# Optimization experiments

Measured on AMD Instinct MI355X. Metric: run time of the kernel, lower is better.

## Reference

```python
import jax, jax.numpy as jnp
import numpy as np

N_NODES = 50000
N_EDGES = 600000
LATENT = 128
IN_FEAT = 7
STEPS = 3
MLP_LAYERS = 2


def setup_inputs() -> dict:
    key = jax.random.key(0)
    ks = jax.random.split(key, 8)
    s = 0.05
    nodes = jax.random.normal(ks[0], (N_NODES, IN_FEAT), jnp.float32)
    senders = jax.random.randint(ks[1], (N_EDGES,), 0, N_NODES, jnp.int32)
    receivers = jax.random.randint(ks[2], (N_EDGES,), 0, N_NODES, jnp.int32)
    W_embed = jax.random.normal(ks[3], (IN_FEAT, LATENT), jnp.float32) * s
    b_embed = jnp.zeros((LATENT,), jnp.float32)
    mlp_W = jax.random.normal(ks[4], (STEPS, MLP_LAYERS, LATENT, LATENT), jnp.float32) * s
    mlp_b = jnp.zeros((STEPS, MLP_LAYERS, LATENT), jnp.float32)
    ln_scale = jnp.ones((STEPS, LATENT), jnp.float32)
    ln_bias = jnp.zeros((STEPS, LATENT), jnp.float32)
    W_dec = jax.random.normal(ks[5], (LATENT, IN_FEAT), jnp.float32) * s
    b_dec = jnp.zeros((IN_FEAT,), jnp.float32)
    return dict(nodes=nodes, senders=senders, receivers=receivers,
                W_embed=W_embed, b_embed=b_embed, mlp_W=mlp_W, mlp_b=mlp_b,
                ln_scale=ln_scale, ln_bias=ln_bias, W_dec=W_dec, b_dec=b_dec)


def _layer_norm(x, scale, bias, eps=1e-6):
    mu = jnp.mean(x, axis=-1, keepdims=True)
    var = jnp.var(x, axis=-1, keepdims=True)
    return (x - mu) * jax.lax.rsqrt(var + eps) * scale + bias


def reference(nodes, senders, receivers, W_embed, b_embed, mlp_W, mlp_b,
              ln_scale, ln_bias, W_dec, b_dec):
    n = nodes.shape[0]
    # symmetric normalization factors (jraph GraphConvolution default)
    ones = jnp.ones((senders.shape[0],), dtype=nodes.dtype)
    sender_deg = jax.ops.segment_sum(ones, senders, num_segments=n)
    receiver_deg = jax.ops.segment_sum(ones, receivers, num_segments=n)
    inv_sqrt_s = jax.lax.rsqrt(jnp.maximum(sender_deg, 1.0))[:, None]
    inv_sqrt_r = jax.lax.rsqrt(jnp.maximum(receiver_deg, 1.0))[:, None]

    # node embedder
    h = nodes @ W_embed + b_embed  # [N, LATENT]
    for step in range(mlp_W.shape[0]):
        # per-node MLP update (update_node_fn applied before aggregation)
        x = h
        for l in range(mlp_W.shape[1]):
            x = jax.nn.relu(x @ mlp_W[step, l] + mlp_b[step, l])
        # normalized gather -> scatter-sum aggregation
        x = x * inv_sqrt_s
        x = jax.ops.segment_sum(x[senders], receivers, num_segments=n)
        x = x * inv_sqrt_r
        # skip connection + layer norm
        h = _layer_norm(h + x, ln_scale[step], ln_bias[step])
    # decoder back to input feature size
    return h @ W_dec + b_dec  # [N, IN_FEAT]
```

## Files before the change

kernel.cpp:

```cpp
#include <hip/hip_runtime.h>

#define NN 50000
#define NE 600000
#define LAT 128
#define IN_F 7
#define CSR_W 64
#define HSTR 136
#define NXCD 8
#define RNG (NN / NXCD)

typedef __attribute__((ext_vector_type(8))) short bfrag;
typedef __attribute__((ext_vector_type(4))) float ffrag;
typedef __attribute__((ext_vector_type(2))) float f32x2;

__device__ inline unsigned short f2bf(float f) {
    unsigned int u = __float_as_uint(f);
    return (unsigned short)((u + 0x7FFFu + ((u >> 16) & 1u)) >> 16);
}
__device__ inline float bf2f(unsigned int b) { return __uint_as_float(b << 16); }


__global__ void k_prep(const float* __restrict__ W, unsigned short* __restrict__ Wp,
                       unsigned int* __restrict__ cnt) {
    int t = blockIdx.x * 256 + threadIdx.x;
    if (t < NN) cnt[t] = 0;
    if (t < 6 * 8 * 4 * 64) {
        int lane = t & 63;
        int ks = (t >> 6) & 3;
        int nt = (t >> 8) & 7;
        int mat = t >> 11;
        int n = nt * 16 + (lane & 15);
        int k0 = ks * 32 + (lane >> 4) * 8;
        const float* src = W + (size_t)mat * LAT * LAT;
        unsigned long long lo = 0, hi = 0;
#pragma unroll
        for (int j = 0; j < 4; ++j)
            lo |= (unsigned long long)f2bf(src[(k0 + j) * LAT + n]) << (16 * j);
#pragma unroll
        for (int j = 0; j < 4; ++j)
            hi |= (unsigned long long)f2bf(src[(k0 + 4 + j) * LAT + n]) << (16 * j);
        unsigned long long* dst = (unsigned long long*)(Wp + (size_t)t * 8);
        dst[0] = lo; dst[1] = hi;
    }
}


__global__ __launch_bounds__(256) void k_fused1(
    const int* __restrict__ s, const int* __restrict__ r,
    unsigned int* __restrict__ cnt, unsigned short* __restrict__ slot,
    const float* __restrict__ nodes, const float* __restrict__ We,
    const float* __restrict__ be,
    const unsigned short* __restrict__ W0p, const unsigned short* __restrict__ W1p,
    const float* __restrict__ b0, const float* __restrict__ b1,
    unsigned char* __restrict__ x, int build_blocks)
{
    __shared__ unsigned short hs[64][HSTR];
    int tid = threadIdx.x;

    if ((int)blockIdx.x < build_blocks) {
        int g = blockIdx.x & (NXCD - 1);
        int stripe = blockIdx.x >> 3;
        int i = stripe * 256 + tid;
        if (i < NE) {
            int ss = s[i], rr = r[i];
            int rlo = g * RNG;
            if (ss >= rlo && ss < rlo + RNG)
                atomicAdd(&cnt[ss], 1u);
            if (rr >= rlo && rr < rlo + RNG) {
                unsigned int p = atomicAdd(&cnt[rr], 0x10000u) >> 16;
                if (p < CSR_W) slot[(size_t)rr * CSR_W + p] = (unsigned short)ss;
            }
        }
        return;
    }

    int brow = ((int)blockIdx.x - build_blocks) * 64;
    int rows = NN - brow; if (rows > 64) rows = 64;

#pragma unroll
    for (int it = 0; it < 8; ++it) {
        int fi = it * 256 + tid;
        int rr = fi >> 5, cc = (fi & 31) << 2;
        if (rr < rows) {
            const float* nr = nodes + (size_t)(brow + rr) * IN_F;
            float o0 = be[cc], o1 = be[cc + 1], o2 = be[cc + 2], o3 = be[cc + 3];
#pragma unroll
            for (int k = 0; k < IN_F; ++k) {
                float nv = nr[k];
                const float* wk = We + k * LAT + cc;
                o0 += nv * wk[0]; o1 += nv * wk[1];
                o2 += nv * wk[2]; o3 += nv * wk[3];
            }
            unsigned long long pk = (unsigned long long)f2bf(o0)
                | ((unsigned long long)f2bf(o1) << 16)
                | ((unsigned long long)f2bf(o2) << 32)
                | ((unsigned long long)f2bf(o3) << 48);
            *(unsigned long long*)&hs[rr][cc] = pk;
        }
    }
    __syncthreads();

    int w = tid >> 6, lane = tid & 63;
    int mrow = w * 16 + (lane & 15);
    int koff = (lane >> 4) * 8;
    int ccol = lane & 15;
    int crow = w * 16 + (lane >> 4) * 4;

    float bia0[8], bia1[8];
#pragma unroll
    for (int nt = 0; nt < 8; ++nt) { bia0[nt] = b0[nt * 16 + ccol]; bia1[nt] = b1[nt * 16 + ccol]; }

    ffrag acc[8];
#pragma unroll
    for (int nt = 0; nt < 8; ++nt) acc[nt] = (ffrag)0.0f;
#pragma unroll
    for (int ks = 0; ks < 4; ++ks) {
        bfrag af = *(const bfrag*)&hs[mrow][ks * 32 + koff];
#pragma unroll
        for (int nt = 0; nt < 8; ++nt) {
            bfrag bf = *(const bfrag*)&W0p[(size_t)(((nt * 4) + ks) * 64 + lane) * 8];
            acc[nt] = __builtin_amdgcn_mfma_f32_16x16x32_bf16(af, bf, acc[nt], 0, 0, 0);
        }
    }
#pragma unroll
    for (int nt = 0; nt < 8; ++nt)
#pragma unroll
        for (int reg = 0; reg < 4; ++reg)
            hs[crow + reg][nt * 16 + ccol] = f2bf(fmaxf(acc[nt][reg] + bia0[nt], 0.f));
    __syncthreads();

#pragma unroll
    for (int nt = 0; nt < 8; ++nt) acc[nt] = (ffrag)0.0f;
#pragma unroll
    for (int ks = 0; ks < 4; ++ks) {
        bfrag af = *(const bfrag*)&hs[mrow][ks * 32 + koff];
#pragma unroll
        for (int nt = 0; nt < 8; ++nt) {
            bfrag bf = *(const bfrag*)&W1p[(size_t)(((nt * 4) + ks) * 64 + lane) * 8];
            acc[nt] = __builtin_amdgcn_mfma_f32_16x16x32_bf16(af, bf, acc[nt], 0, 0, 0);
        }
    }
    __syncthreads();
#pragma unroll
    for (int nt = 0; nt < 8; ++nt)
#pragma unroll
        for (int reg = 0; reg < 4; ++reg)
            hs[crow + reg][nt * 16 + ccol] = f2bf(fmaxf(acc[nt][reg] + bia1[nt], 0.f));
    __syncthreads();

#pragma unroll
    for (int it = 0; it < 8; ++it) {
        int fi = it * 256 + tid;
        int rr = fi >> 5, uc = fi & 31;
        if (rr < rows) {
            unsigned long long pk8 = *(unsigned long long*)&hs[rr][uc * 4];
            float f0 = bf2f((unsigned int)(pk8 & 0xFFFFu));
            float f1 = bf2f((unsigned int)((pk8 >> 16) & 0xFFFFu));
            float f2 = bf2f((unsigned int)((pk8 >> 32) & 0xFFFFu));
            float f3 = bf2f((unsigned int)((pk8 >> 48) & 0xFFFFu));
            int o = __builtin_amdgcn_cvt_pk_fp8_f32(f0, f1, 0, false);
            o = __builtin_amdgcn_cvt_pk_fp8_f32(f2, f3, o, true);
            *(int*)&x[(size_t)(brow + rr) * LAT + uc * 4] = o;
        }
    }
}


__global__ __launch_bounds__(256) void k_mlp2(
    const unsigned short* __restrict__ h,
    const unsigned short* __restrict__ W0p, const unsigned short* __restrict__ W1p,
    const float* __restrict__ b0, const float* __restrict__ b1,
    const unsigned int* __restrict__ cnt,
    unsigned char* __restrict__ x, int M)
{
    __shared__ unsigned short hs[64][HSTR];
    int brow = blockIdx.x * 64;
    int tid = threadIdx.x;
    int rows = M - brow; if (rows > 64) rows = 64;

#pragma unroll
    for (int it = 0; it < 8; ++it) {
        int fi = it * 256 + tid;
        int rr = fi >> 5, cc = (fi & 31) << 2;
        if (rr < rows)
            *(unsigned long long*)&hs[rr][cc] =
                *(const unsigned long long*)&h[(size_t)(brow + rr) * LAT + cc];
    }
    __syncthreads();

    int w = tid >> 6, lane = tid & 63;
    int mrow = w * 16 + (lane & 15);
    int koff = (lane >> 4) * 8;
    int ccol = lane & 15;
    int crow = w * 16 + (lane >> 4) * 4;

    float bia0[8], bia1[8];
#pragma unroll
    for (int nt = 0; nt < 8; ++nt) { bia0[nt] = b0[nt * 16 + ccol]; bia1[nt] = b1[nt * 16 + ccol]; }
    float iv[4];
#pragma unroll
    for (int reg = 0; reg < 4; ++reg) {
        int rw = brow + crow + reg;
        unsigned int ds = cnt[rw < NN ? rw : NN - 1] & 0xFFFFu;
        iv[reg] = rsqrtf((float)(ds > 1 ? ds : 1));
    }

    ffrag acc[8];
#pragma unroll
    for (int nt = 0; nt < 8; ++nt) acc[nt] = (ffrag)0.0f;
#pragma unroll
    for (int ks = 0; ks < 4; ++ks) {
        bfrag af = *(const bfrag*)&hs[mrow][ks * 32 + koff];
#pragma unroll
        for (int nt = 0; nt < 8; ++nt) {
            bfrag bf = *(const bfrag*)&W0p[(size_t)(((nt * 4) + ks) * 64 + lane) * 8];
            acc[nt] = __builtin_amdgcn_mfma_f32_16x16x32_bf16(af, bf, acc[nt], 0, 0, 0);
        }
    }
#pragma unroll
    for (int nt = 0; nt < 8; ++nt)
#pragma unroll
        for (int reg = 0; reg < 4; ++reg)
            hs[crow + reg][nt * 16 + ccol] = f2bf(fmaxf(acc[nt][reg] + bia0[nt], 0.f));
    __syncthreads();

#pragma unroll
    for (int nt = 0; nt < 8; ++nt) acc[nt] = (ffrag)0.0f;
#pragma unroll
    for (int ks = 0; ks < 4; ++ks) {
        bfrag af = *(const bfrag*)&hs[mrow][ks * 32 + koff];
#pragma unroll
        for (int nt = 0; nt < 8; ++nt) {
            bfrag bf = *(const bfrag*)&W1p[(size_t)(((nt * 4) + ks) * 64 + lane) * 8];
            acc[nt] = __builtin_amdgcn_mfma_f32_16x16x32_bf16(af, bf, acc[nt], 0, 0, 0);
        }
    }
    __syncthreads();
#pragma unroll
    for (int nt = 0; nt < 8; ++nt)
#pragma unroll
        for (int reg = 0; reg < 4; ++reg)
            hs[crow + reg][nt * 16 + ccol] =
                f2bf(fmaxf(acc[nt][reg] + bia1[nt], 0.f) * iv[reg]);
    __syncthreads();

#pragma unroll
    for (int it = 0; it < 8; ++it) {
        int fi = it * 256 + tid;
        int rr = fi >> 5, uc = fi & 31;
        if (rr < rows) {
            unsigned long long pk8 = *(unsigned long long*)&hs[rr][uc * 4];
            float f0 = bf2f((unsigned int)(pk8 & 0xFFFFu));
            float f1 = bf2f((unsigned int)((pk8 >> 16) & 0xFFFFu));
            float f2 = bf2f((unsigned int)((pk8 >> 32) & 0xFFFFu));
            float f3 = bf2f((unsigned int)((pk8 >> 48) & 0xFFFFu));
            int o = __builtin_amdgcn_cvt_pk_fp8_f32(f0, f1, 0, false);
            o = __builtin_amdgcn_cvt_pk_fp8_f32(f2, f3, o, true);
            *(int*)&x[(size_t)(brow + rr) * LAT + uc * 4] = o;
        }
    }
}


__global__ __launch_bounds__(256) void k_agg(
    const unsigned char* __restrict__ x, unsigned short* __restrict__ h,
    const float* __restrict__ nodes, const float* __restrict__ We,
    const float* __restrict__ be,
    const unsigned int* __restrict__ cnt, const unsigned short* __restrict__ slot,
    const float* __restrict__ gamma, const float* __restrict__ beta,
    const float* __restrict__ Wd, const float* __restrict__ bd,
    float* __restrict__ outd, int mode)
{
    int lane = threadIdx.x & 63;
    int r = blockIdx.x * 4 + (threadIdx.x >> 6);
    if (r >= NN) return;

    int ct = (int)(cnt[r] >> 16);
    float ir = rsqrtf((float)(ct > 1 ? ct : 1));
    int c = ct > CSR_W ? CSR_W : ct;

    int myidx = (lane < c) ? (int)slot[(size_t)r * CSR_W + lane] : 0;

    int j0 = lane * 2;
    float ax0 = 0.f, ay0 = 0.f, ax1 = 0.f, ay1 = 0.f;
    float ax2 = 0.f, ay2 = 0.f, ax3 = 0.f, ay3 = 0.f;
    float ax4 = 0.f, ay4 = 0.f, ax5 = 0.f, ay5 = 0.f;
    float ax6 = 0.f, ay6 = 0.f, ax7 = 0.f, ay7 = 0.f;
    int e = 0;

    if (mode == 0) {
        float myinv = 0.f;
        if (lane < c) {
            unsigned int ds = cnt[myidx] & 0xFFFFu;
            myinv = rsqrtf((float)(ds > 1 ? ds : 1));
        }
        for (; e + 8 <= c; e += 8) {
            int s0 = __shfl(myidx, e),     s1 = __shfl(myidx, e + 1);
            int s2 = __shfl(myidx, e + 2), s3 = __shfl(myidx, e + 3);
            int s4 = __shfl(myidx, e + 4), s5 = __shfl(myidx, e + 5);
            int s6 = __shfl(myidx, e + 6), s7 = __shfl(myidx, e + 7);
            float w0 = __shfl(myinv, e),     w1 = __shfl(myinv, e + 1);
            float w2 = __shfl(myinv, e + 2), w3 = __shfl(myinv, e + 3);
            float w4 = __shfl(myinv, e + 4), w5 = __shfl(myinv, e + 5);
            float w6 = __shfl(myinv, e + 6), w7 = __shfl(myinv, e + 7);
            unsigned short v0 = *(const unsigned short*)&x[(size_t)s0 * LAT + j0];
            unsigned short v1 = *(const unsigned short*)&x[(size_t)s1 * LAT + j0];
            unsigned short v2 = *(const unsigned short*)&x[(size_t)s2 * LAT + j0];
            unsigned short v3 = *(const unsigned short*)&x[(size_t)s3 * LAT + j0];
            unsigned short v4 = *(const unsigned short*)&x[(size_t)s4 * LAT + j0];
            unsigned short v5 = *(const unsigned short*)&x[(size_t)s5 * LAT + j0];
            unsigned short v6 = *(const unsigned short*)&x[(size_t)s6 * LAT + j0];
            unsigned short v7 = *(const unsigned short*)&x[(size_t)s7 * LAT + j0];
            f32x2 d0 = __builtin_amdgcn_cvt_pk_f32_fp8((int)v0, false);
            f32x2 d1 = __builtin_amdgcn_cvt_pk_f32_fp8((int)v1, false);
            f32x2 d2 = __builtin_amdgcn_cvt_pk_f32_fp8((int)v2, false);
            f32x2 d3 = __builtin_amdgcn_cvt_pk_f32_fp8((int)v3, false);
            f32x2 d4 = __builtin_amdgcn_cvt_pk_f32_fp8((int)v4, false);
            f32x2 d5 = __builtin_amdgcn_cvt_pk_f32_fp8((int)v5, false);
            f32x2 d6 = __builtin_amdgcn_cvt_pk_f32_fp8((int)v6, false);
            f32x2 d7 = __builtin_amdgcn_cvt_pk_f32_fp8((int)v7, false);
            ax0 += d0.x * w0; ay0 += d0.y * w0;
            ax1 += d1.x * w1; ay1 += d1.y * w1;
            ax2 += d2.x * w2; ay2 += d2.y * w2;
            ax3 += d3.x * w3; ay3 += d3.y * w3;
            ax4 += d4.x * w4; ay4 += d4.y * w4;
            ax5 += d5.x * w5; ay5 += d5.y * w5;
            ax6 += d6.x * w6; ay6 += d6.y * w6;
            ax7 += d7.x * w7; ay7 += d7.y * w7;
        }
        for (; e < c; ++e) {
            int s0 = __shfl(myidx, e);
            float w0 = __shfl(myinv, e);
            unsigned short v0 = *(const unsigned short*)&x[(size_t)s0 * LAT + j0];
            f32x2 d0 = __builtin_amdgcn_cvt_pk_f32_fp8((int)v0, false);
            ax0 += d0.x * w0; ay0 += d0.y * w0;
        }
    } else {
        for (; e + 8 <= c; e += 8) {
            int s0 = __shfl(myidx, e),     s1 = __shfl(myidx, e + 1);
            int s2 = __shfl(myidx, e + 2), s3 = __shfl(myidx, e + 3);
            int s4 = __shfl(myidx, e + 4), s5 = __shfl(myidx, e + 5);
            int s6 = __shfl(myidx, e + 6), s7 = __shfl(myidx, e + 7);
            unsigned short v0 = *(const unsigned short*)&x[(size_t)s0 * LAT + j0];
            unsigned short v1 = *(const unsigned short*)&x[(size_t)s1 * LAT + j0];
            unsigned short v2 = *(const unsigned short*)&x[(size_t)s2 * LAT + j0];
            unsigned short v3 = *(const unsigned short*)&x[(size_t)s3 * LAT + j0];
            unsigned short v4 = *(const unsigned short*)&x[(size_t)s4 * LAT + j0];
            unsigned short v5 = *(const unsigned short*)&x[(size_t)s5 * LAT + j0];
            unsigned short v6 = *(const unsigned short*)&x[(size_t)s6 * LAT + j0];
            unsigned short v7 = *(const unsigned short*)&x[(size_t)s7 * LAT + j0];
            f32x2 d0 = __builtin_amdgcn_cvt_pk_f32_fp8((int)v0, false);
            f32x2 d1 = __builtin_amdgcn_cvt_pk_f32_fp8((int)v1, false);
            f32x2 d2 = __builtin_amdgcn_cvt_pk_f32_fp8((int)v2, false);
            f32x2 d3 = __builtin_amdgcn_cvt_pk_f32_fp8((int)v3, false);
            f32x2 d4 = __builtin_amdgcn_cvt_pk_f32_fp8((int)v4, false);
            f32x2 d5 = __builtin_amdgcn_cvt_pk_f32_fp8((int)v5, false);
            f32x2 d6 = __builtin_amdgcn_cvt_pk_f32_fp8((int)v6, false);
            f32x2 d7 = __builtin_amdgcn_cvt_pk_f32_fp8((int)v7, false);
            ax0 += d0.x; ay0 += d0.y;  ax1 += d1.x; ay1 += d1.y;
            ax2 += d2.x; ay2 += d2.y;  ax3 += d3.x; ay3 += d3.y;
            ax4 += d4.x; ay4 += d4.y;  ax5 += d5.x; ay5 += d5.y;
            ax6 += d6.x; ay6 += d6.y;  ax7 += d7.x; ay7 += d7.y;
        }
        for (; e < c; ++e) {
            int s0 = __shfl(myidx, e);
            unsigned short v0 = *(const unsigned short*)&x[(size_t)s0 * LAT + j0];
            f32x2 d0 = __builtin_amdgcn_cvt_pk_f32_fp8((int)v0, false);
            ax0 += d0.x; ay0 += d0.y;
        }
    }

    float a0 = (((ax0 + ax1) + (ax2 + ax3)) + ((ax4 + ax5) + (ax6 + ax7))) * ir;
    float a1 = (((ay0 + ay1) + (ay2 + ay3)) + ((ay4 + ay5) + (ay6 + ay7))) * ir;

    float v0, v1;
    if (mode == 0) {
        float o0 = be[j0], o1 = be[j0 + 1];
#pragma unroll
        for (int k = 0; k < IN_F; ++k) {
            float nv = nodes[(size_t)r * IN_F + k];
            o0 += nv * We[k * LAT + j0];
            o1 += nv * We[k * LAT + j0 + 1];
        }
        v0 = o0 + a0; v1 = o1 + a1;
    } else {
        unsigned int hv = *(const unsigned int*)&h[(size_t)r * LAT + j0];
        v0 = bf2f(hv & 0xFFFFu) + a0;
        v1 = bf2f(hv >> 16) + a1;
    }

    float sum = v0 + v1, sq = v0 * v0 + v1 * v1;
#pragma unroll
    for (int m = 1; m <= 32; m <<= 1) {
        sum += __shfl_xor(sum, m);
        sq  += __shfl_xor(sq, m);
    }
    float mu = sum * (1.f / LAT);
    float rs = rsqrtf(sq * (1.f / LAT) - mu * mu + 1e-6f);

    float o0 = (v0 - mu) * rs * gamma[j0] + beta[j0];
    float o1 = (v1 - mu) * rs * gamma[j0 + 1] + beta[j0 + 1];

    if (mode < 2) {
        *(unsigned int*)&h[(size_t)r * LAT + j0] =
            (unsigned int)f2bf(o0) | ((unsigned int)f2bf(o1) << 16);
    } else {
        const float* wd0 = Wd + j0 * IN_F;
        const float* wd1 = Wd + (j0 + 1) * IN_F;
#pragma unroll
        for (int f = 0; f < IN_F; ++f) {
            float pv = o0 * wd0[f] + o1 * wd1[f];
#pragma unroll
            for (int m = 1; m <= 32; m <<= 1) pv += __shfl_xor(pv, m);
            if (lane == 0) outd[(size_t)r * IN_F + f] = pv + bd[f];
        }
    }
}


extern "C" void kernel_launch(void* const* d_in, const int* in_sizes, int n_in,
                              void* d_out, int out_size, void* d_ws, size_t ws_size,
                              hipStream_t stream)
{
    const float* nodes   = (const float*)d_in[0];
    const int*   senders = (const int*)d_in[1];
    const int*   recvs   = (const int*)d_in[2];
    const float* W_embed = (const float*)d_in[3];
    const float* b_embed = (const float*)d_in[4];
    const float* mlp_W   = (const float*)d_in[5];
    const float* mlp_b   = (const float*)d_in[6];
    const float* ln_s    = (const float*)d_in[7];
    const float* ln_b    = (const float*)d_in[8];
    const float* W_dec   = (const float*)d_in[9];
    const float* b_dec   = (const float*)d_in[10];
    float* out = (float*)d_out;

    char* p = (char*)d_ws;
    auto alloc = [&](size_t bytes) -> char* {
        char* q = p; p += (bytes + 255) & ~(size_t)255; return q;
    };
    unsigned short* h    = (unsigned short*)alloc((size_t)NN * LAT * 2);
    unsigned char*  x    = (unsigned char*)alloc((size_t)NN * LAT);
    unsigned short* Wp   = (unsigned short*)alloc((size_t)6 * LAT * LAT * 2);
    unsigned int* cnt    = (unsigned int*)alloc((size_t)NN * 4);
    unsigned short* slot = (unsigned short*)alloc((size_t)NN * CSR_W * 2);

    k_prep<<<(NN + 255) / 256, 256, 0, stream>>>(mlp_W, Wp, cnt);

    int build_blocks = NXCD * ((NE + 255) / 256);
    int mlp_blocks   = (NN + 63) / 64;
    int agg_blocks   = (NN + 3) / 4;

    const float* b0 = mlp_b;
    k_fused1<<<build_blocks + mlp_blocks, 256, 0, stream>>>(
        senders, recvs, cnt, slot, nodes, W_embed, b_embed,
        Wp, Wp + (size_t)LAT * LAT, b0, b0 + LAT, x, build_blocks);

    k_agg<<<agg_blocks, 256, 0, stream>>>(
        x, h, nodes, W_embed, b_embed, cnt, slot,
        ln_s, ln_b, nullptr, nullptr, nullptr, 0);

    k_mlp2<<<mlp_blocks, 256, 0, stream>>>(
        h, Wp + (size_t)2 * LAT * LAT, Wp + (size_t)3 * LAT * LAT,
        b0 + 2 * LAT, b0 + 3 * LAT, cnt, x, NN);
    k_agg<<<agg_blocks, 256, 0, stream>>>(
        x, h, nodes, W_embed, b_embed, cnt, slot,
        ln_s + LAT, ln_b + LAT, nullptr, nullptr, nullptr, 1);

    k_mlp2<<<mlp_blocks, 256, 0, stream>>>(
        h, Wp + (size_t)4 * LAT * LAT, Wp + (size_t)5 * LAT * LAT,
        b0 + 4 * LAT, b0 + 5 * LAT, cnt, x, NN);
    k_agg<<<agg_blocks, 256, 0, stream>>>(
        x, h, nodes, W_embed, b_embed, cnt, slot,
        ln_s + 2 * LAT, ln_b + 2 * LAT, W_dec, b_dec, out, 2);
}
```

Baseline: 315.1 us.

## Process two nodes per wavefront in aggregation with 4-byte fp8 gathers

Restructures the aggregation/layernorm kernel so each 64-lane wavefront handles two destination nodes, 32 lanes each, with every lane gathering 4 fp8 features (a 4-byte load) instead of 2 (a 2-byte load). Edge indices and weights are held in two registers per lane and broadcast with shuffles; the edge loop runs to the larger degree of the paired nodes and zero-weights missing entries. The goal is fewer, wider gather transactions per edge and half the wavefronts. In exchange, work is wasted when the paired degrees differ, and the early return for out-of-range rows is gone, which is safe only because NN is divisible by 8.

```diff
diff --git a/kernel.cpp b/kernel.cpp
--- a/kernel.cpp
+++ b/kernel.cpp
@@ -271,148 +271,110 @@
     const float* __restrict__ Wd, const float* __restrict__ bd,
     float* __restrict__ outd, int mode)
 {
-    int lane = threadIdx.x & 63;
-    int r = blockIdx.x * 4 + (threadIdx.x >> 6);
-    if (r >= NN) return;
+    int tid = threadIdx.x;
+    int wid = tid >> 6;
+    int lane = tid & 63;
+    int half = lane >> 5;
+    int li = lane & 31;
+    int r = blockIdx.x * 8 + wid * 2 + half;
+    int cb = li * 4;
 
     int ct = (int)(cnt[r] >> 16);
     float ir = rsqrtf((float)(ct > 1 ? ct : 1));
     int c = ct > CSR_W ? CSR_W : ct;
 
-    int myidx = (lane < c) ? (int)slot[(size_t)r * CSR_W + lane] : 0;
-
-    int j0 = lane * 2;
-    float ax0 = 0.f, ay0 = 0.f, ax1 = 0.f, ay1 = 0.f;
-    float ax2 = 0.f, ay2 = 0.f, ax3 = 0.f, ay3 = 0.f;
-    float ax4 = 0.f, ay4 = 0.f, ax5 = 0.f, ay5 = 0.f;
-    float ax6 = 0.f, ay6 = 0.f, ax7 = 0.f, ay7 = 0.f;
-    int e = 0;
-
+    int idx0 = 0, idx1 = 0;
+    float wt0 = 0.f, wt1 = 0.f;
+    if (li < c)      idx0 = (int)slot[(size_t)r * CSR_W + li];
+    if (32 + li < c) idx1 = (int)slot[(size_t)r * CSR_W + 32 + li];
     if (mode == 0) {
-        float myinv = 0.f;
-        if (lane < c) {
-            unsigned int ds = cnt[myidx] & 0xFFFFu;
-            myinv = rsqrtf((float)(ds > 1 ? ds : 1));
-        }
-        for (; e + 8 <= c; e += 8) {
-            int s0 = __shfl(myidx, e),     s1 = __shfl(myidx, e + 1);
-            int s2 = __shfl(myidx, e + 2), s3 = __shfl(myidx, e + 3);
-            int s4 = __shfl(myidx, e + 4), s5 = __shfl(myidx, e + 5);
-            int s6 = __shfl(myidx, e + 6), s7 = __shfl(myidx, e + 7);
-            float w0 = __shfl(myinv, e),     w1 = __shfl(myinv, e + 1);
-            float w2 = __shfl(myinv, e + 2), w3 = __shfl(myinv, e + 3);
-            float w4 = __shfl(myinv, e + 4), w5 = __shfl(myinv, e + 5);
-            float w6 = __shfl(myinv, e + 6), w7 = __shfl(myinv, e + 7);
-            unsigned short v0 = *(const unsigned short*)&x[(size_t)s0 * LAT + j0];
-            unsigned short v1 = *(const unsigned short*)&x[(size_t)s1 * LAT + j0];
-            unsigned short v2 = *(const unsigned short*)&x[(size_t)s2 * LAT + j0];
-            unsigned short v3 = *(const unsigned short*)&x[(size_t)s3 * LAT + j0];
-            unsigned short v4 = *(const unsigned short*)&x[(size_t)s4 * LAT + j0];
-            unsigned short v5 = *(const unsigned short*)&x[(size_t)s5 * LAT + j0];
-            unsigned short v6 = *(const unsigned short*)&x[(size_t)s6 * LAT + j0];
-            unsigned short v7 = *(const unsigned short*)&x[(size_t)s7 * LAT + j0];
-            f32x2 d0 = __builtin_amdgcn_cvt_pk_f32_fp8((int)v0, false);
-            f32x2 d1 = __builtin_amdgcn_cvt_pk_f32_fp8((int)v1, false);
-            f32x2 d2 = __builtin_amdgcn_cvt_pk_f32_fp8((int)v2, false);
-            f32x2 d3 = __builtin_amdgcn_cvt_pk_f32_fp8((int)v3, false);
-            f32x2 d4 = __builtin_amdgcn_cvt_pk_f32_fp8((int)v4, false);
-            f32x2 d5 = __builtin_amdgcn_cvt_pk_f32_fp8((int)v5, false);
-            f32x2 d6 = __builtin_amdgcn_cvt_pk_f32_fp8((int)v6, false);
-            f32x2 d7 = __builtin_amdgcn_cvt_pk_f32_fp8((int)v7, false);
-            ax0 += d0.x * w0; ay0 += d0.y * w0;
-            ax1 += d1.x * w1; ay1 += d1.y * w1;
-            ax2 += d2.x * w2; ay2 += d2.y * w2;
-            ax3 += d3.x * w3; ay3 += d3.y * w3;
-            ax4 += d4.x * w4; ay4 += d4.y * w4;
-            ax5 += d5.x * w5; ay5 += d5.y * w5;
-            ax6 += d6.x * w6; ay6 += d6.y * w6;
-            ax7 += d7.x * w7; ay7 += d7.y * w7;
-        }
-        for (; e < c; ++e) {
-            int s0 = __shfl(myidx, e);
-            float w0 = __shfl(myinv, e);
-            unsigned short v0 = *(const unsigned short*)&x[(size_t)s0 * LAT + j0];
-            f32x2 d0 = __builtin_amdgcn_cvt_pk_f32_fp8((int)v0, false);
-            ax0 += d0.x * w0; ay0 += d0.y * w0;
-        }
+        if (li < c)      { unsigned int d = cnt[idx0] & 0xFFFFu; wt0 = rsqrtf((float)(d > 1 ? d : 1)); }
+        if (32 + li < c) { unsigned int d = cnt[idx1] & 0xFFFFu; wt1 = rsqrtf((float)(d > 1 ? d : 1)); }
     } else {
-        for (; e + 8 <= c; e += 8) {
-            int s0 = __shfl(myidx, e),     s1 = __shfl(myidx, e + 1);
-            int s2 = __shfl(myidx, e + 2), s3 = __shfl(myidx, e + 3);
-            int s4 = __shfl(myidx, e + 4), s5 = __shfl(myidx, e + 5);
-            int s6 = __shfl(myidx, e + 6), s7 = __shfl(myidx, e + 7);
-            unsigned short v0 = *(const unsigned short*)&x[(size_t)s0 * LAT + j0];
-            unsigned short v1 = *(const unsigned short*)&x[(size_t)s1 * LAT + j0];
-            unsigned short v2 = *(const unsigned short*)&x[(size_t)s2 * LAT + j0];
-            unsigned short v3 = *(const unsigned short*)&x[(size_t)s3 * LAT + j0];
-            unsigned short v4 = *(const unsigned short*)&x[(size_t)s4 * LAT + j0];
-            unsigned short v5 = *(const unsigned short*)&x[(size_t)s5 * LAT + j0];
-            unsigned short v6 = *(const unsigned short*)&x[(size_t)s6 * LAT + j0];
-            unsigned short v7 = *(const unsigned short*)&x[(size_t)s7 * LAT + j0];
-            f32x2 d0 = __builtin_amdgcn_cvt_pk_f32_fp8((int)v0, false);
-            f32x2 d1 = __builtin_amdgcn_cvt_pk_f32_fp8((int)v1, false);
-            f32x2 d2 = __builtin_amdgcn_cvt_pk_f32_fp8((int)v2, false);
-            f32x2 d3 = __builtin_amdgcn_cvt_pk_f32_fp8((int)v3, false);
-            f32x2 d4 = __builtin_amdgcn_cvt_pk_f32_fp8((int)v4, false);
-            f32x2 d5 = __builtin_amdgcn_cvt_pk_f32_fp8((int)v5, false);
-            f32x2 d6 = __builtin_amdgcn_cvt_pk_f32_fp8((int)v6, false);
-            f32x2 d7 = __builtin_amdgcn_cvt_pk_f32_fp8((int)v7, false);
-            ax0 += d0.x; ay0 += d0.y;  ax1 += d1.x; ay1 += d1.y;
-            ax2 += d2.x; ay2 += d2.y;  ax3 += d3.x; ay3 += d3.y;
-            ax4 += d4.x; ay4 += d4.y;  ax5 += d5.x; ay5 += d5.y;
-            ax6 += d6.x; ay6 += d6.y;  ax7 += d7.x; ay7 += d7.y;
-        }
-        for (; e < c; ++e) {
-            int s0 = __shfl(myidx, e);
-            unsigned short v0 = *(const unsigned short*)&x[(size_t)s0 * LAT + j0];
-            f32x2 d0 = __builtin_amdgcn_cvt_pk_f32_fp8((int)v0, false);
-            ax0 += d0.x; ay0 += d0.y;
-        }
-    }
-
-    float a0 = (((ax0 + ax1) + (ax2 + ax3)) + ((ax4 + ax5) + (ax6 + ax7))) * ir;
-    float a1 = (((ay0 + ay1) + (ay2 + ay3)) + ((ay4 + ay5) + (ay6 + ay7))) * ir;
-
-    float v0, v1;
+        wt0 = (li < c) ? 1.f : 0.f;
+        wt1 = (32 + li < c) ? 1.f : 0.f;
+    }
+
+    int cother = __shfl_xor(c, 32);
+    int cmax = c > cother ? c : cother;
+
+    float ac[4][4];
+#pragma unroll
+    for (int k = 0; k < 4; ++k)
+#pragma unroll
+        for (int j = 0; j < 4; ++j) ac[k][j] = 0.f;
+
+    int base = half * 32;
+    for (int e = 0; e < cmax; e += 4) {
+#pragma unroll
+        for (int k = 0; k < 4; ++k) {
+            int ee = e + k;
+            int srcl = base + (ee & 31);
+            int idx  = __shfl(ee < 32 ? idx0 : idx1, srcl);
+            float wv = __shfl(ee < 32 ? wt0 : wt1, srcl);
+            unsigned int v = *(const unsigned int*)&x[(size_t)idx * LAT + cb];
+            f32x2 dlo = __builtin_amdgcn_cvt_pk_f32_fp8((int)v, false);
+            f32x2 dhi = __builtin_amdgcn_cvt_pk_f32_fp8((int)v, true);
+            ac[k][0] += dlo.x * wv; ac[k][1] += dlo.y * wv;
+            ac[k][2] += dhi.x * wv; ac[k][3] += dhi.y * wv;
+        }
+    }
+
+    float sagg[4];
+#pragma unroll
+    for (int j = 0; j < 4; ++j)
+        sagg[j] = ((ac[0][j] + ac[1][j]) + (ac[2][j] + ac[3][j])) * ir;
+
+    float val[4];
     if (mode == 0) {
-        float o0 = be[j0], o1 = be[j0 + 1];
-#pragma unroll
-        for (int k = 0; k < IN_F; ++k) {
-            float nv = nodes[(size_t)r * IN_F + k];
-            o0 += nv * We[k * LAT + j0];
-            o1 += nv * We[k * LAT + j0 + 1];
-        }
-        v0 = o0 + a0; v1 = o1 + a1;
+        float nk[IN_F];
+#pragma unroll
+        for (int k = 0; k < IN_F; ++k) nk[k] = nodes[(size_t)r * IN_F + k];
+#pragma unroll
+        for (int j = 0; j < 4; ++j) {
+            float o = be[cb + j];
+#pragma unroll
+            for (int k = 0; k < IN_F; ++k) o += nk[k] * We[k * LAT + cb + j];
+            val[j] = o + sagg[j];
+        }
     } else {
-        unsigned int hv = *(const unsigned int*)&h[(size_t)r * LAT + j0];
-        v0 = bf2f(hv & 0xFFFFu) + a0;
-        v1 = bf2f(hv >> 16) + a1;
-    }
-
-    float sum = v0 + v1, sq = v0 * v0 + v1 * v1;
-#pragma unroll
-    for (int m = 1; m <= 32; m <<= 1) {
+        uint2 hv = *(const uint2*)&h[(size_t)r * LAT + cb];
+        val[0] = bf2f(hv.x & 0xFFFFu) + sagg[0];
+        val[1] = bf2f(hv.x >> 16)     + sagg[1];
+        val[2] = bf2f(hv.y & 0xFFFFu) + sagg[2];
+        val[3] = bf2f(hv.y >> 16)     + sagg[3];
+    }
+
+    float sum = 0.f, sq = 0.f;
+#pragma unroll
+    for (int j = 0; j < 4; ++j) { sum += val[j]; sq += val[j] * val[j]; }
+#pragma unroll
+    for (int m = 1; m <= 16; m <<= 1) {
         sum += __shfl_xor(sum, m);
         sq  += __shfl_xor(sq, m);
     }
     float mu = sum * (1.f / LAT);
     float rs = rsqrtf(sq * (1.f / LAT) - mu * mu + 1e-6f);
 
-    float o0 = (v0 - mu) * rs * gamma[j0] + beta[j0];
-    float o1 = (v1 - mu) * rs * gamma[j0 + 1] + beta[j0 + 1];
+    float o[4];
+#pragma unroll
+    for (int j = 0; j < 4; ++j)
+        o[j] = (val[j] - mu) * rs * gamma[cb + j] + beta[cb + j];
 
     if (mode < 2) {
-        *(unsigned int*)&h[(size_t)r * LAT + j0] =
-            (unsigned int)f2bf(o0) | ((unsigned int)f2bf(o1) << 16);
+        uint2 st;
+        st.x = (unsigned int)f2bf(o[0]) | ((unsigned int)f2bf(o[1]) << 16);
+        st.y = (unsigned int)f2bf(o[2]) | ((unsigned int)f2bf(o[3]) << 16);
+        *(uint2*)&h[(size_t)r * LAT + cb] = st;
     } else {
-        const float* wd0 = Wd + j0 * IN_F;
-        const float* wd1 = Wd + (j0 + 1) * IN_F;
 #pragma unroll
         for (int f = 0; f < IN_F; ++f) {
-            float pv = o0 * wd0[f] + o1 * wd1[f];
-#pragma unroll
-            for (int m = 1; m <= 32; m <<= 1) pv += __shfl_xor(pv, m);
-            if (lane == 0) outd[(size_t)r * IN_F + f] = pv + bd[f];
+            float pv = 0.f;
+#pragma unroll
+            for (int j = 0; j < 4; ++j) pv += o[j] * Wd[(cb + j) * IN_F + f];
+#pragma unroll
+            for (int m = 1; m <= 16; m <<= 1) pv += __shfl_xor(pv, m);
+            if (li == 0) outd[(size_t)r * IN_F + f] = pv + bd[f];
         }
     }
 }
@@ -449,7 +411,7 @@
 
     int build_blocks = NXCD * ((NE + 255) / 256);
     int mlp_blocks   = (NN + 63) / 64;
-    int agg_blocks   = (NN + 3) / 4;
+    int agg_blocks   = (NN + 7) / 8;
 
     const float* b0 = mlp_b;
     k_fused1<<<build_blocks + mlp_blocks, 256, 0, stream>>>(
```

Result: faster. 294.0 us (-6.7%).
